# Performance work log

Measured on AMD Instinct MI355X. Metric: run time of the kernel, lower is better.

## Reference

```python
import jax, jax.numpy as jnp
import numpy as np

SCALES = [2 ** i for i in range(11)]  # init: scales=10 -> [1,2,...,1024]
B, N, C, K = 8, 1024, 256, 4096


def setup_inputs() -> dict:
    key = jax.random.key(0)
    k1, k2, k3 = jax.random.split(key, 3)
    f_BNC = jax.random.normal(k1, (B, N, C), dtype=jnp.float32)
    base = jax.random.normal(k2, (K, C), dtype=jnp.float32)          # orthogonal-init codebook base
    proj_w = jax.random.normal(k3, (C, C), dtype=jnp.float32) / np.float32(np.sqrt(C))  # xavier-ish
    proj_b = jnp.zeros((C,), dtype=jnp.float32)
    return {"f_BNC": f_BNC, "base": base, "proj_w": proj_w, "proj_b": proj_b}


def _linear_interp(x, out_size):
    # x: [B, C, n] -> [B, C, out_size], matches F.interpolate(mode='linear', align_corners=False)
    n = x.shape[-1]
    scale = n / out_size
    src = jnp.maximum((jnp.arange(out_size, dtype=jnp.float32) + 0.5) * scale - 0.5, 0.0)
    i0 = jnp.floor(src).astype(jnp.int32)
    i1 = jnp.minimum(i0 + 1, n - 1)
    w = (src - i0.astype(jnp.float32)).astype(x.dtype)
    return x[..., i0] * (1.0 - w) + x[..., i1] * w


def reference(f_BNC, base, proj_w, proj_b):
    sg = jax.lax.stop_gradient
    # update_embedding(): embedding = proj(base)
    embedding = base @ proj_w.T + proj_b                 # [K, C]
    emb_ng = sg(embedding)
    e_sq = jnp.sum(emb_ng * emb_ng, axis=1)              # [K]

    f_BCN = jnp.transpose(f_BNC, (0, 2, 1))              # [B, C, N]
    f_ng = sg(f_BCN)
    f_rest = f_ng
    f_hat = jnp.zeros_like(f_ng)
    commit = jnp.float32(0.0)
    qlat = jnp.float32(0.0)
    SN = len(SCALES)

    for pn in SCALES:
        # area interpolation == exact mean pooling since N % pn == 0
        rest_BCp = f_rest.reshape(B, C, pn, N // pn).mean(axis=-1)       # [B, C, pn]
        q = jnp.transpose(rest_BCp, (0, 2, 1)).reshape(-1, C)            # [B*pn, C]
        # squared-distance to codebook (gradients never flow through d: argmin only)
        d = jnp.sum(q * q, axis=1, keepdims=True) + e_sq - 2.0 * (q @ emb_ng.T)  # [B*pn, K]
        idx = jnp.argmin(d, axis=1)                                      # [B*pn]
        h_BnC = embedding[idx].reshape(B, pn, C)                         # gather (grad flows to codebook)
        h_BCn = _linear_interp(jnp.transpose(h_BnC, (0, 2, 1)), N)       # [B, C, N]
        f_hat = f_hat + h_BCn
        # residual feeds only argmin at the next scale -> dead gradient path in torch too
        f_rest = f_rest - sg(h_BCn)
        commit = commit + 0.25 * jnp.mean((sg(f_hat) - f_BCN) ** 2)
        qlat = qlat + jnp.mean((f_hat - f_ng) ** 2)

    commit = commit / SN
    qlat = qlat / SN
    # straight-through: f_hat = (f_hat.data - f_no_grad) + f_BCN
    f_out = sg(f_hat) - f_ng + f_BCN
    return (jnp.transpose(f_out, (0, 2, 1)), commit, qlat)
```

## Files before the change

### kernel.cpp

```cpp
#include <hip/hip_runtime.h>
#include <cfloat>

#define BB 8
#define NN 1024
#define CC 256
#define KK 4096
#define SN 11
#define BNC (BB*NN*CC)
#define RMAX 8192

typedef __attribute__((ext_vector_type(8))) _Float16 half8;
typedef __attribute__((ext_vector_type(4))) float f32x4;

__device__ __forceinline__ void split2(float v, ushort& h, ushort& l) {
    union { _Float16 f; ushort u; } a, b;
    a.f = (_Float16)v;
    b.f = (_Float16)(v - (float)a.f);
    h = a.u; l = b.u;
}

__global__ void transpose_pw(const float* __restrict__ pw, float* __restrict__ pwT) {
    int j = blockIdx.x;
    int c = threadIdx.x;
    pwT[j * CC + c] = pw[c * CC + j];
}

__global__ __launch_bounds__(256) void embed_kernel(
    const float* __restrict__ base, const float* __restrict__ pwT,
    const float* __restrict__ pb, float* __restrict__ emb,
    ushort* __restrict__ eh, ushort* __restrict__ el, float* __restrict__ esq) {
    __shared__ float bs[16][CC];
    __shared__ float wpart[16][4];
    int k0 = blockIdx.x * 16;
    int t = threadIdx.x;
    int w = t >> 6, lane = t & 63;
    for (int i = t; i < 16 * CC; i += 256) bs[i >> 8][i & 255] = base[k0 * CC + i];
    __syncthreads();
    float acc[16];
#pragma unroll
    for (int m = 0; m < 16; ++m) acc[m] = 0.f;
    for (int j = 0; j < CC; ++j) {
        float wv = pwT[j * CC + t];
#pragma unroll
        for (int m = 0; m < 16; ++m) acc[m] += bs[m][j] * wv;
    }
    float bias = pb[t];
#pragma unroll
    for (int m = 0; m < 16; ++m) {
        float v = acc[m] + bias;
        int o = (k0 + m) * CC + t;
        emb[o] = v;
        ushort h, l;
        split2(64.f * v, h, l);
        eh[o] = h; el[o] = l;
        float sq = v * v;
#pragma unroll
        for (int d = 1; d < 64; d <<= 1) sq += __shfl_xor(sq, d);
        if (lane == 0) wpart[m][w] = sq;
    }
    __syncthreads();
    if (t < 16) esq[k0 + t] = wpart[t][0] + wpart[t][1] + wpart[t][2] + wpart[t][3];
}

__global__ __launch_bounds__(256) void init_pool16(const float* __restrict__ f,
                                                   float* __restrict__ p16) {
    int blk = blockIdx.x;
    int t = threadIdx.x;
    size_t base = (size_t)blk * 16 * CC + t;
    float s = 0.f;
#pragma unroll
    for (int j = 0; j < 16; ++j) s += f[base + (size_t)j * CC];
    p16[(size_t)blk * CC + t] = s;
}

__global__ void poolB(const float* __restrict__ p16, float* __restrict__ qf, int pnn) {
    int r = blockIdx.x;
    int b = r / pnn, p = r - b * pnn;
    int g16 = 64 / pnn;
    int c4 = threadIdx.x;
    const float4* src = (const float4*)(p16 + ((size_t)b * 64 + (size_t)p * g16) * CC) + c4;
    float4 s = make_float4(0.f, 0.f, 0.f, 0.f);
    for (int i = 0; i < g16; ++i) {
        float4 v = src[(size_t)i * 64];
        s.x += v.x; s.y += v.y; s.z += v.z; s.w += v.w;
    }
    float inv = 1.f / (float)(g16 * 16);
    s.x *= inv; s.y *= inv; s.z *= inv; s.w *= inv;
    ((float4*)(qf + (size_t)r * CC))[c4] = s;
}

__global__ __launch_bounds__(256, 4) void dist_small(
    const float* __restrict__ qf, const float* __restrict__ emb,
    const float* __restrict__ esq, int R,
    float* __restrict__ pval, int* __restrict__ pidx) {
    __shared__ float qs[32][CC];
    __shared__ float es[64][33];
    int t = threadIdx.x;
    int ws = t >> 6, j = t & 63;
    int k0 = blockIdx.x * 64;
    int r0c = blockIdx.y * 32;
    {
        int row = t >> 3, c0 = (t & 7) * 32;
        int gr = r0c + row;
#pragma unroll
        for (int i = 0; i < 8; ++i) {
            float4 v = (gr < R) ? *(const float4*)&qf[(size_t)gr * CC + c0 + 4 * i]
                                : make_float4(0.f, 0.f, 0.f, 0.f);
            *(float4*)&qs[row][c0 + 4 * i] = v;
        }
    }
    float acc[8];
#pragma unroll
    for (int ri = 0; ri < 8; ++ri) acc[ri] = 0.f;
    for (int ck = 0; ck < 8; ++ck) {
        __syncthreads();
        {
            int code = t >> 2, cb = (t & 3) * 8;
            float4 v0 = *(const float4*)&emb[(size_t)(k0 + code) * CC + ck * 32 + cb];
            float4 v1 = *(const float4*)&emb[(size_t)(k0 + code) * CC + ck * 32 + cb + 4];
            es[code][cb + 0] = v0.x; es[code][cb + 1] = v0.y;
            es[code][cb + 2] = v0.z; es[code][cb + 3] = v0.w;
            es[code][cb + 4] = v1.x; es[code][cb + 5] = v1.y;
            es[code][cb + 6] = v1.z; es[code][cb + 7] = v1.w;
        }
        __syncthreads();
        for (int c = 0; c < 32; ++c) {
            float ev = es[j][c];
#pragma unroll
            for (int ri = 0; ri < 8; ++ri)
                acc[ri] += qs[ws + 4 * ri][ck * 32 + c] * ev;
        }
    }
    float esv = esq[k0 + j];
#pragma unroll
    for (int ri = 0; ri < 8; ++ri) {
        int r = r0c + ws + 4 * ri;
        if (r >= R) continue;
        float v = esv - 2.f * acc[ri];
        int bi = k0 + j;
#pragma unroll
        for (int d = 1; d < 64; d <<= 1) {
            float ov = __shfl_xor(v, d);
            int oi = __shfl_xor(bi, d);
            if (ov < v || (ov == v && oi < bi)) { v = ov; bi = oi; }
        }
        if (j == 0) {
            pval[(size_t)r * 64 + blockIdx.x] = v;
            pidx[(size_t)r * 64 + blockIdx.x] = bi;
        }
    }
}

__global__ __launch_bounds__(256, 2) void dist_mfma(
    const ushort* __restrict__ qh, const ushort* __restrict__ ql,
    const ushort* __restrict__ eh, const ushort* __restrict__ el,
    const float* __restrict__ esq,
    float* __restrict__ pval, int* __restrict__ pidx) {
    __shared__ ushort tiles[4096 * 8];
    __shared__ float wv[2][128];
    __shared__ int wi[2][128];
    int t = threadIdx.x;
    int w = t >> 6, lane = t & 63;
    int l15 = lane & 15, hi = lane >> 4;
    int wr = w >> 1, wc = w & 1;
    int r0 = blockIdx.x * 128;
    int kb = blockIdx.y;
    int k0 = kb * 128;

    f32x4 acc[4][4];
#pragma unroll
    for (int mi = 0; mi < 4; ++mi)
#pragma unroll
        for (int ni = 0; ni < 4; ++ni) acc[mi][ni] = (f32x4){0.f, 0.f, 0.f, 0.f};

    for (int ck = 0; ck < 4; ++ck) {
        __syncthreads();
#pragma unroll
        for (int it = 0; it < 16; ++it) {
            int s = it * 256 + t;
            const ushort* g;
            if (s < 2048) {
                int a = s >> 10;
                int rem = s & 1023;
                int row = rem >> 3, sr = rem & 7;
                int c = (ck << 6) + ((sr ^ (row & 7)) << 3);
                g = (a ? ql : qh) + (size_t)(r0 + row) * CC + c;
            } else {
                int s2 = s - 2048;
                int b = s2 >> 10;
                int rem = s2 & 1023;
                int kcol = rem >> 3, sr = rem & 7;
                int c = (ck << 6) + ((sr ^ (kcol & 7)) << 3);
                g = (b ? el : eh) + (size_t)(k0 + kcol) * CC + c;
            }
            ushort* lb = &tiles[(size_t)(it * 256 + (w << 6)) * 8];
            __builtin_amdgcn_global_load_lds(
                (const __attribute__((address_space(1))) unsigned int*)g,
                (__attribute__((address_space(3))) unsigned int*)lb, 16, 0, 0);
        }
        __syncthreads();

#pragma unroll
        for (int kk = 0; kk < 2; ++kk) {
            int cs = (kk << 2) + hi;
            half8 bf0[4], bf1[4], af[4];
#pragma unroll
            for (int ni = 0; ni < 4; ++ni) {
                int kcol = (wc << 6) + (ni << 4) + l15;
                int sb = 2048 + (kcol << 3) + (cs ^ (kcol & 7));
                bf0[ni] = *(const half8*)&tiles[sb * 8];
                bf1[ni] = *(const half8*)&tiles[(sb + 1024) * 8];
            }
#pragma unroll
            for (int mi = 0; mi < 4; ++mi) {
                int row = (wr << 6) + (mi << 4) + l15;
                af[mi] = *(const half8*)&tiles[((row << 3) + (cs ^ (row & 7))) * 8];
            }
#pragma unroll
            for (int mi = 0; mi < 4; ++mi)
#pragma unroll
                for (int ni = 0; ni < 4; ++ni)
                    acc[mi][ni] = __builtin_amdgcn_mfma_f32_16x16x32_f16(af[mi], bf0[ni], acc[mi][ni], 0, 0, 0);
#pragma unroll
            for (int mi = 0; mi < 4; ++mi)
#pragma unroll
                for (int ni = 0; ni < 4; ++ni)
                    acc[mi][ni] = __builtin_amdgcn_mfma_f32_16x16x32_f16(af[mi], bf1[ni], acc[mi][ni], 0, 0, 0);
#pragma unroll
            for (int mi = 0; mi < 4; ++mi) {
                int row = (wr << 6) + (mi << 4) + l15;
                af[mi] = *(const half8*)&tiles[(1024 + (row << 3) + (cs ^ (row & 7))) * 8];
            }
#pragma unroll
            for (int mi = 0; mi < 4; ++mi)
#pragma unroll
                for (int ni = 0; ni < 4; ++ni)
                    acc[mi][ni] = __builtin_amdgcn_mfma_f32_16x16x32_f16(af[mi], bf0[ni], acc[mi][ni], 0, 0, 0);
        }
    }

    int cbase = k0 + (wc << 6) + l15;
    float es4[4];
#pragma unroll
    for (int ni = 0; ni < 4; ++ni) es4[ni] = 4096.f * esq[cbase + ni * 16];
#pragma unroll
    for (int mi = 0; mi < 4; ++mi) {
#pragma unroll
        for (int reg = 0; reg < 4; ++reg) {
            float v = es4[0] - 2.f * acc[mi][0][reg];
            int i = cbase;
#pragma unroll
            for (int ni = 1; ni < 4; ++ni) {
                float v1 = es4[ni] - 2.f * acc[mi][ni][reg];
                if (v1 < v) { v = v1; i = cbase + ni * 16; }
            }
#pragma unroll
            for (int d = 1; d < 16; d <<= 1) {
                float ov = __shfl_xor(v, d);
                int oi = __shfl_xor(i, d);
                if (ov < v || (ov == v && oi < i)) { v = ov; i = oi; }
            }
            if (l15 == 0) {
                int row = (wr << 6) + (mi << 4) + (hi << 2) + reg;
                wv[wc][row] = v;
                wi[wc][row] = i;
            }
        }
    }
    __syncthreads();
    if (t < 128) {
        float v = wv[0][t];
        int i = wi[0][t];
        float ov = wv[1][t];
        int oi = wi[1][t];
        if (ov < v || (ov == v && oi < i)) { v = ov; i = oi; }
        pval[(size_t)(r0 + t) * 64 + kb] = v;
        pidx[(size_t)(r0 + t) * 64 + kb] = i;
    }
}

__global__ __launch_bounds__(256) void update_pool(
    const float* __restrict__ emb, const float* __restrict__ pval,
    const int* __restrict__ pidx, const float* __restrict__ f,
    float* __restrict__ fhat, float* __restrict__ parts,
    ushort* __restrict__ qh, ushort* __restrict__ ql,
    float* __restrict__ qf, float* __restrict__ p16u,
    int pn, int gn, int pnn, int ks) {
    int blk = blockIdx.x;
    int b = blk >> 6, n16 = blk & 63;
    int t = threadIdx.x;
    int w = t >> 6, lane = t & 63;
    int n0 = n16 * 16;
    const float scale = (float)pn * (1.0f / 1024.0f);
    float s_lo = (n0 + 0.5f) * scale - 0.5f;
    if (s_lo < 0.f) s_lo = 0.f;
    int r_lo = (int)s_lo;
    float s_hi = (n0 + 15.5f) * scale - 0.5f;
    if (s_hi < 0.f) s_hi = 0.f;
    int r_hi = min((int)s_hi + 1, pn - 1);
    int cnt = r_hi - r_lo + 1;
    __shared__ int sidx[20];
    for (int ri = w; ri < cnt; ri += 4) {
        size_t rowg = (size_t)(b * pn + r_lo + ri) * 64;
        float v = (lane < ks) ? pval[rowg + lane] : FLT_MAX;
        int i = (lane < ks) ? pidx[rowg + lane] : 0x7fffffff;
#pragma unroll
        for (int d = 1; d < 64; d <<= 1) {
            float ov = __shfl_xor(v, d);
            int oi = __shfl_xor(i, d);
            if (ov < v || (ov == v && oi < i)) { v = ov; i = oi; }
        }
        if (lane == 0) sidx[ri] = i;
    }
    __syncthreads();
    float sq = 0.f;
    float pr = 0.f;
    for (int j = 0; j < 16; ++j) {
        int n = n0 + j;
        float s = (n + 0.5f) * scale - 0.5f;
        if (s < 0.f) s = 0.f;
        int i0 = (int)s;
        float wgt = s - (float)i0;
        int i1 = min(i0 + 1, pn - 1);
        int k0 = sidx[i0 - r_lo];
        int k1 = sidx[i1 - r_lo];
        float e0 = emb[(size_t)k0 * CC + t];
        float e1 = emb[(size_t)k1 * CC + t];
        float h = (1.f - wgt) * e0 + wgt * e1;
        size_t o = ((size_t)b * NN + n) * CC + t;
        float fh = fhat[o] + h;
        fhat[o] = fh;
        float fv = f[o];
        float d = fh - fv;
        sq += d * d;
        pr += (fv - fh);
        if (gn > 0 && gn < 16 && ((j & (gn - 1)) == (gn - 1))) {
            float mean = pr * (1.f / (float)gn);
            ushort H, L;
            split2(64.f * mean, H, L);
            size_t r = (size_t)b * pnn + (size_t)(n / gn);
            qh[r * CC + t] = H;
            ql[r * CC + t] = L;
            pr = 0.f;
        }
    }
    if (gn == 16) qf[(size_t)blk * CC + t] = pr * (1.f / 16.f);
    else if (gn >= 32) p16u[(size_t)blk * CC + t] = pr;
    for (int off = 32; off > 0; off >>= 1) sq += __shfl_down(sq, off);
    __shared__ float wred[4];
    if (lane == 0) wred[w] = sq;
    __syncthreads();
    if (t == 0) parts[blk] = wred[0] + wred[1] + wred[2] + wred[3];
}

__global__ void reduce_final(const float* __restrict__ parts, float* __restrict__ out) {
    __shared__ float red[256];
    int t = threadIdx.x;
    float s = 0.f;
    for (int i = t; i < SN * 512; i += 256) s += parts[i];
    red[t] = s;
    __syncthreads();
    for (int k = 128; k > 0; k >>= 1) {
        if (t < k) red[t] += red[t + k];
        __syncthreads();
    }
    if (t == 0) {
        float mean_sum = red[0] / (float)BNC;
        out[BNC] = 0.25f * mean_sum / (float)SN;
        out[BNC + 1] = mean_sum / (float)SN;
    }
}

extern "C" void kernel_launch(void* const* d_in, const int* in_sizes, int n_in,
                              void* d_out, int out_size, void* d_ws, size_t ws_size,
                              hipStream_t stream) {
    const float* f    = (const float*)d_in[0];
    const float* base = (const float*)d_in[1];
    const float* pw   = (const float*)d_in[2];
    const float* pb   = (const float*)d_in[3];
    float* out = (float*)d_out;

    float* emb   = (float*)d_ws;
    float* esq   = emb + (size_t)KK * CC;
    float* pwT   = esq + KK;
    float* parts = pwT + (size_t)CC * CC;
    float* pval  = parts + (size_t)SN * 512;
    float* p16   = pval + (size_t)RMAX * 64;
    float* p16u  = p16 + (size_t)BB * 64 * CC;
    float* qf    = p16u + (size_t)BB * 64 * CC;
    int*   pidx  = (int*)(qf + (size_t)512 * CC);
    ushort* eh = (ushort*)(pidx + (size_t)RMAX * 64);
    ushort* el = eh + (size_t)KK * CC;
    ushort* qh = el + (size_t)KK * CC;
    ushort* ql = qh + (size_t)RMAX * CC;

    hipMemsetAsync(out, 0, (size_t)BNC * sizeof(float), stream);

    transpose_pw<<<CC, CC, 0, stream>>>(pw, pwT);
    embed_kernel<<<KK / 16, 256, 0, stream>>>(base, pwT, pb, emb, eh, el, esq);
    init_pool16<<<BB * 64, 256, 0, stream>>>(f, p16);
    poolB<<<8, 64, 0, stream>>>(p16, qf, 1);

    for (int sidx = 0; sidx < SN; ++sidx) {
        int pn = 1 << sidx;
        int R = BB * pn;
        int ks;
        if (pn <= 64) {
            dim3 grid(64, (R + 31) / 32);
            dist_small<<<grid, 256, 0, stream>>>(qf, emb, esq, R, pval, pidx);
            ks = 64;
        } else {
            dist_mfma<<<dim3(R / 128, 32), 256, 0, stream>>>(qh, ql, eh, el, esq, pval, pidx);
            ks = 32;
        }
        int pnn = (sidx < SN - 1) ? (pn << 1) : 0;
        int gn = pnn ? (NN / pnn) : 0;
        update_pool<<<BB * 64, 256, 0, stream>>>(emb, pval, pidx, f, out,
                                                 parts + (size_t)sidx * 512,
                                                 qh, ql, qf, p16u, pn, gn, pnn, ks);
        if (pnn && gn >= 32) poolB<<<BB * pnn, 64, 0, stream>>>(p16u, qf, pnn);
    }
    reduce_final<<<1, 256, 0, stream>>>(parts, out);
}
```

Before: 560.9 us.

## Load MFMA operands directly from global and track residual instead of f_hat

The distance MFMA kernel drops its LDS staging tiles and barriers. Each wave now reads its fp16 hi/lo operand fragments straight from global memory, and the occupancy hint rises from 2 to 3 blocks. Separately, the update kernel keeps a running residual buffer (f - f_hat) in place of f_hat. This removes the extra read of f at every scale and the initial memset of the output, and the output is written only at the final scale. The global-load path gives up LDS reuse across waves and relies on L1/L2 to absorb the duplicate fragment loads.

```diff
diff --git a/kernel.cpp b/kernel.cpp
--- a/kernel.cpp
+++ b/kernel.cpp
@@ -151,12 +151,11 @@
     }
 }
 
-__global__ __launch_bounds__(256, 2) void dist_mfma(
+__global__ __launch_bounds__(256, 3) void dist_mfma(
     const ushort* __restrict__ qh, const ushort* __restrict__ ql,
     const ushort* __restrict__ eh, const ushort* __restrict__ el,
     const float* __restrict__ esq,
     float* __restrict__ pval, int* __restrict__ pidx) {
-    __shared__ ushort tiles[4096 * 8];
     __shared__ float wv[2][128];
     __shared__ int wi[2][128];
     int t = threadIdx.x;
@@ -167,76 +166,48 @@
     int kb = blockIdx.y;
     int k0 = kb * 128;
 
+    size_t aoff = (size_t)(r0 + (wr << 6) + l15) * CC + (hi << 3);
+    size_t boff = (size_t)(k0 + (wc << 6) + l15) * CC + (hi << 3);
+    const ushort* pah = qh + aoff;
+    const ushort* pal = ql + aoff;
+    const ushort* pbh = eh + boff;
+    const ushort* pbl = el + boff;
+
     f32x4 acc[4][4];
 #pragma unroll
     for (int mi = 0; mi < 4; ++mi)
 #pragma unroll
         for (int ni = 0; ni < 4; ++ni) acc[mi][ni] = (f32x4){0.f, 0.f, 0.f, 0.f};
 
-    for (int ck = 0; ck < 4; ++ck) {
-        __syncthreads();
-#pragma unroll
-        for (int it = 0; it < 16; ++it) {
-            int s = it * 256 + t;
-            const ushort* g;
-            if (s < 2048) {
-                int a = s >> 10;
-                int rem = s & 1023;
-                int row = rem >> 3, sr = rem & 7;
-                int c = (ck << 6) + ((sr ^ (row & 7)) << 3);
-                g = (a ? ql : qh) + (size_t)(r0 + row) * CC + c;
-            } else {
-                int s2 = s - 2048;
-                int b = s2 >> 10;
-                int rem = s2 & 1023;
-                int kcol = rem >> 3, sr = rem & 7;
-                int c = (ck << 6) + ((sr ^ (kcol & 7)) << 3);
-                g = (b ? el : eh) + (size_t)(k0 + kcol) * CC + c;
-            }
-            ushort* lb = &tiles[(size_t)(it * 256 + (w << 6)) * 8];
-            __builtin_amdgcn_global_load_lds(
-                (const __attribute__((address_space(1))) unsigned int*)g,
-                (__attribute__((address_space(3))) unsigned int*)lb, 16, 0, 0);
-        }
-        __syncthreads();
-
-#pragma unroll
-        for (int kk = 0; kk < 2; ++kk) {
-            int cs = (kk << 2) + hi;
-            half8 bf0[4], bf1[4], af[4];
-#pragma unroll
-            for (int ni = 0; ni < 4; ++ni) {
-                int kcol = (wc << 6) + (ni << 4) + l15;
-                int sb = 2048 + (kcol << 3) + (cs ^ (kcol & 7));
-                bf0[ni] = *(const half8*)&tiles[sb * 8];
-                bf1[ni] = *(const half8*)&tiles[(sb + 1024) * 8];
-            }
-#pragma unroll
-            for (int mi = 0; mi < 4; ++mi) {
-                int row = (wr << 6) + (mi << 4) + l15;
-                af[mi] = *(const half8*)&tiles[((row << 3) + (cs ^ (row & 7))) * 8];
-            }
-#pragma unroll
-            for (int mi = 0; mi < 4; ++mi)
-#pragma unroll
-                for (int ni = 0; ni < 4; ++ni)
-                    acc[mi][ni] = __builtin_amdgcn_mfma_f32_16x16x32_f16(af[mi], bf0[ni], acc[mi][ni], 0, 0, 0);
-#pragma unroll
-            for (int mi = 0; mi < 4; ++mi)
-#pragma unroll
-                for (int ni = 0; ni < 4; ++ni)
-                    acc[mi][ni] = __builtin_amdgcn_mfma_f32_16x16x32_f16(af[mi], bf1[ni], acc[mi][ni], 0, 0, 0);
-#pragma unroll
-            for (int mi = 0; mi < 4; ++mi) {
-                int row = (wr << 6) + (mi << 4) + l15;
-                af[mi] = *(const half8*)&tiles[(1024 + (row << 3) + (cs ^ (row & 7))) * 8];
-            }
-#pragma unroll
-            for (int mi = 0; mi < 4; ++mi)
-#pragma unroll
-                for (int ni = 0; ni < 4; ++ni)
-                    acc[mi][ni] = __builtin_amdgcn_mfma_f32_16x16x32_f16(af[mi], bf0[ni], acc[mi][ni], 0, 0, 0);
-        }
+#pragma unroll
+    for (int ks = 0; ks < 8; ++ks) {
+        const int kd = ks << 5;
+        half8 ah[4], al[4], bh[4], bl[4];
+#pragma unroll
+        for (int mi = 0; mi < 4; ++mi) {
+            ah[mi] = *(const half8*)(pah + (size_t)(mi << 4) * CC + kd);
+            al[mi] = *(const half8*)(pal + (size_t)(mi << 4) * CC + kd);
+        }
+#pragma unroll
+        for (int ni = 0; ni < 4; ++ni) {
+            bh[ni] = *(const half8*)(pbh + (size_t)(ni << 4) * CC + kd);
+            bl[ni] = *(const half8*)(pbl + (size_t)(ni << 4) * CC + kd);
+        }
+#pragma unroll
+        for (int mi = 0; mi < 4; ++mi)
+#pragma unroll
+            for (int ni = 0; ni < 4; ++ni)
+                acc[mi][ni] = __builtin_amdgcn_mfma_f32_16x16x32_f16(ah[mi], bh[ni], acc[mi][ni], 0, 0, 0);
+#pragma unroll
+        for (int mi = 0; mi < 4; ++mi)
+#pragma unroll
+            for (int ni = 0; ni < 4; ++ni)
+                acc[mi][ni] = __builtin_amdgcn_mfma_f32_16x16x32_f16(ah[mi], bl[ni], acc[mi][ni], 0, 0, 0);
+#pragma unroll
+        for (int mi = 0; mi < 4; ++mi)
+#pragma unroll
+            for (int ni = 0; ni < 4; ++ni)
+                acc[mi][ni] = __builtin_amdgcn_mfma_f32_16x16x32_f16(al[mi], bh[ni], acc[mi][ni], 0, 0, 0);
     }
 
     int cbase = k0 + (wc << 6) + l15;
@@ -281,11 +252,12 @@
 
 __global__ __launch_bounds__(256) void update_pool(
     const float* __restrict__ emb, const float* __restrict__ pval,
-    const int* __restrict__ pidx, const float* __restrict__ f,
-    float* __restrict__ fhat, float* __restrict__ parts,
+    const int* __restrict__ pidx, const float* __restrict__ rin,
+    float* __restrict__ rout, const float* __restrict__ f,
+    float* __restrict__ outp, float* __restrict__ parts,
     ushort* __restrict__ qh, ushort* __restrict__ ql,
     float* __restrict__ qf, float* __restrict__ p16u,
-    int pn, int gn, int pnn, int ks) {
+    int pn, int gn, int pnn, int ks, int finalflag) {
     int blk = blockIdx.x;
     int b = blk >> 6, n16 = blk & 63;
     int t = threadIdx.x;
@@ -328,12 +300,11 @@
         float e1 = emb[(size_t)k1 * CC + t];
         float h = (1.f - wgt) * e0 + wgt * e1;
         size_t o = ((size_t)b * NN + n) * CC + t;
-        float fh = fhat[o] + h;
-        fhat[o] = fh;
-        float fv = f[o];
-        float d = fh - fv;
-        sq += d * d;
-        pr += (fv - fh);
+        float rv = rin[o] - h;
+        if (!finalflag) rout[o] = rv;
+        else outp[o] = f[o] - rv;
+        sq += rv * rv;
+        pr += rv;
         if (gn > 0 && gn < 16 && ((j & (gn - 1)) == (gn - 1))) {
             float mean = pr * (1.f / (float)gn);
             ushort H, L;
@@ -388,13 +359,12 @@
     float* p16   = pval + (size_t)RMAX * 64;
     float* p16u  = p16 + (size_t)BB * 64 * CC;
     float* qf    = p16u + (size_t)BB * 64 * CC;
-    int*   pidx  = (int*)(qf + (size_t)512 * CC);
+    float* resid = qf + (size_t)512 * CC;
+    int*   pidx  = (int*)(resid + BNC);
     ushort* eh = (ushort*)(pidx + (size_t)RMAX * 64);
     ushort* el = eh + (size_t)KK * CC;
     ushort* qh = el + (size_t)KK * CC;
     ushort* ql = qh + (size_t)RMAX * CC;
-
-    hipMemsetAsync(out, 0, (size_t)BNC * sizeof(float), stream);
 
     transpose_pw<<<CC, CC, 0, stream>>>(pw, pwT);
     embed_kernel<<<KK / 16, 256, 0, stream>>>(base, pwT, pb, emb, eh, el, esq);
@@ -415,9 +385,11 @@
         }
         int pnn = (sidx < SN - 1) ? (pn << 1) : 0;
         int gn = pnn ? (NN / pnn) : 0;
-        update_pool<<<BB * 64, 256, 0, stream>>>(emb, pval, pidx, f, out,
+        const float* rin = (sidx == 0) ? f : resid;
+        update_pool<<<BB * 64, 256, 0, stream>>>(emb, pval, pidx, rin, resid, f, out,
                                                  parts + (size_t)sidx * 512,
-                                                 qh, ql, qf, p16u, pn, gn, pnn, ks);
+                                                 qh, ql, qf, p16u, pn, gn, pnn, ks,
+                                                 (sidx == SN - 1) ? 1 : 0);
         if (pnn && gn >= 32) poolB<<<BB * pnn, 64, 0, stream>>>(p16u, qf, pnn);
     }
     reduce_final<<<1, 256, 0, stream>>>(parts, out);
```

Measured after the change: 667.0 us. 18.9% more time.
